# Kernel tuning notes

Measured on AMD Instinct MI355X. Metric: run time of the kernel, lower is better.

## Reference

```python
import jax, jax.numpy as jnp
import numpy as np

NTOK0, NTOK1 = 2048, 512
EMSIZE = 256
NHID = 1024
B, T = 32, 512


def setup_inputs() -> dict:
    key = jax.random.key(0)
    ks = jax.random.split(key, 12)
    initrange = 0.1
    inp = {
        "tokens0": jax.random.randint(ks[0], (B, T), 0, NTOK0),
        "tokens1": jax.random.randint(ks[1], (B, T), 0, NTOK1),
        "h0": jnp.zeros((B, NHID), jnp.float32),
        "c0": jnp.zeros((B, NHID), jnp.float32),
        # embeddings (uniform init as in init_weights)
        "emb0": jax.random.uniform(ks[2], (NTOK0, EMSIZE), jnp.float32, -initrange, initrange),
        "emb1": jax.random.uniform(ks[3], (NTOK1, EMSIZE), jnp.float32, -initrange, initrange),
        # LSTMCell params (PyTorch layout: gates stacked [i, f, g, o])
        "W_ih": jax.random.normal(ks[4], (4 * NHID, 2 * EMSIZE), jnp.float32) * 0.03,
        "W_hh": jax.random.normal(ks[5], (4 * NHID, NHID), jnp.float32) * 0.03,
        "b_ih": jnp.zeros((4 * NHID,), jnp.float32),
        "b_hh": jnp.zeros((4 * NHID,), jnp.float32),
        # per-channel decoders
        "Wd0": jax.random.uniform(ks[6], (NTOK0, NHID), jnp.float32, -initrange, initrange),
        "bd0": jnp.zeros((NTOK0,), jnp.float32),
        "Wd1": jax.random.uniform(ks[7], (NTOK1, NHID), jnp.float32, -initrange, initrange),
        "bd1": jnp.zeros((NTOK1,), jnp.float32),
    }
    return inp


def _lstm_scan(x_bte, h0, c0, W_ih, W_hh, b_ih, b_hh):
    # x_bte: [B, T, 2*EMSIZE] -> scan over time
    def step(carry, x_t):
        h, c = carry
        gates = x_t @ W_ih.T + b_ih + h @ W_hh.T + b_hh  # [B, 4*NHID]
        i, f, g, o = jnp.split(gates, 4, axis=-1)
        i = jax.nn.sigmoid(i)
        f = jax.nn.sigmoid(f)
        g = jnp.tanh(g)
        o = jax.nn.sigmoid(o)
        c = f * c + i * g
        h = o * jnp.tanh(c)
        return (h, c), h

    (h, c), hs = jax.lax.scan(step, (h0, c0), jnp.transpose(x_bte, (1, 0, 2)))
    return jnp.transpose(hs, (1, 0, 2)), h, c  # [B, T, NHID]


def reference(tokens0, tokens1, h0, c0, emb0, emb1, W_ih, W_hh, b_ih, b_hh, Wd0, bd0, Wd1, bd1):
    # encode each channel and concat along feature dim (dropout=0 / eval mode)
    x = jnp.concatenate([emb0[tokens0], emb1[tokens1]], axis=-1)  # [B, T, 2*EMSIZE]
    hs, h_t, c_t = _lstm_scan(x, h0, c0, W_ih, W_hh, b_ih, b_hh)
    dec0 = hs @ Wd0.T + bd0  # [B, T, NTOK0]
    dec1 = hs @ Wd1.T + bd1  # [B, T, NTOK1]
    return dec0, dec1, h_t, c_t
```

## Files before the change

### kernel.cpp

```cpp
#include <hip/hip_runtime.h>

#define DI __device__ __forceinline__

typedef __attribute__((ext_vector_type(8))) short s16x8;
typedef __attribute__((ext_vector_type(4))) float f32x4;

constexpr int BB = 32, TT = 512, NH = 1024, NG = 4096, KX = 512, KT = 1536;
constexpr int NT0 = 2048, NT1 = 512;

constexpr size_t OFF_DEC1 = (size_t)BB * TT * NT0;
constexpr size_t OFF_H    = OFF_DEC1 + (size_t)BB * TT * NT1;
constexpr size_t OFF_C    = OFF_H + (size_t)BB * NH;

constexpr size_t WS_WCAT = 0;
constexpr size_t WS_WD0  = WS_WCAT + (size_t)NG * KT * 2;
constexpr size_t WS_WD1  = WS_WD0 + (size_t)NT0 * NH * 2;
constexpr size_t WS_XE   = WS_WD1 + (size_t)NT1 * NH * 2;
constexpr size_t WS_HSX  = WS_XE + (size_t)TT * BB * KX * 2;
constexpr size_t WS_BIAS = WS_HSX + (size_t)(TT + 1) * BB * NH * 2;
constexpr size_t WS_CNT  = WS_BIAS + (size_t)NG * 4;

DI unsigned short f2bf(float f) {
  unsigned u = __float_as_uint(f);
  u += 0x7fffu + ((u >> 16) & 1u);
  return (unsigned short)(u >> 16);
}

DI s16x8 load16_cp(const unsigned short* p) {
  s16x8 d;
  asm volatile("global_load_dwordx4 %0, %1, off sc0 sc1" : "=v"(d) : "v"(p) : "memory");
  return d;
}
DI void store4_cp(unsigned* p, unsigned v) {
  asm volatile("global_store_dword %0, %1, off sc0 sc1" :: "v"(p), "v"(v) : "memory");
}


__global__ __launch_bounds__(256) void k_wcat(const float* __restrict__ Wih,
                                              const float* __restrict__ Whh,
                                              unsigned short* __restrict__ Wcat) {
  int n = blockIdx.x;
  for (int k = threadIdx.x; k < KT; k += 256) {
    float v = (k < KX) ? Wih[(size_t)n * KX + k] : Whh[(size_t)n * NH + (k - KX)];
    Wcat[(size_t)n * KT + k] = f2bf(v);
  }
}

__global__ __launch_bounds__(256) void k_wd(const float* __restrict__ Wd0,
                                            const float* __restrict__ Wd1,
                                            unsigned short* __restrict__ Wd0b,
                                            unsigned short* __restrict__ Wd1b) {
  int bid = blockIdx.x;
  const float* src;
  unsigned short* dst;
  if (bid < NT0) { src = Wd0 + (size_t)bid * NH; dst = Wd0b + (size_t)bid * NH; }
  else           { src = Wd1 + (size_t)(bid - NT0) * NH; dst = Wd1b + (size_t)(bid - NT0) * NH; }
  for (int k = threadIdx.x; k < NH; k += 256) dst[k] = f2bf(src[k]);
}

__global__ __launch_bounds__(256) void k_misc(const float* __restrict__ bih,
                                              const float* __restrict__ bhh,
                                              const float* __restrict__ h0,
                                              float* __restrict__ bias,
                                              unsigned short* __restrict__ hsx,
                                              unsigned* __restrict__ cnt) {
  int i = blockIdx.x * 256 + threadIdx.x;
  if (i < NG) bias[i] = bih[i] + bhh[i];
  else if (i < NG + BB * NH) { int j = i - NG; hsx[j] = f2bf(h0[j]); }
  else if (i == NG + BB * NH) *cnt = 0u;
}

__global__ __launch_bounds__(64) void k_embed(const int* __restrict__ tok0,
                                              const int* __restrict__ tok1,
                                              const float* __restrict__ emb0,
                                              const float* __restrict__ emb1,
                                              unsigned short* __restrict__ xe) {
  int r = blockIdx.x;
  int t = r >> 5, b = r & 31;
  int i = threadIdx.x;
  int a0 = tok0[b * TT + t], a1 = tok1[b * TT + t];
  const float4* e0 = (const float4*)(emb0 + (size_t)a0 * 256);
  const float4* e1 = (const float4*)(emb1 + (size_t)a1 * 256);
  float4 v0 = e0[i], v1 = e1[i];
  unsigned short* dst = xe + (size_t)r * KX;
  dst[i * 4 + 0] = f2bf(v0.x); dst[i * 4 + 1] = f2bf(v0.y);
  dst[i * 4 + 2] = f2bf(v0.z); dst[i * 4 + 3] = f2bf(v0.w);
  dst[256 + i * 4 + 0] = f2bf(v1.x); dst[256 + i * 4 + 1] = f2bf(v1.y);
  dst[256 + i * 4 + 2] = f2bf(v1.z); dst[256 + i * 4 + 3] = f2bf(v1.w);
}

__global__ __launch_bounds__(256, 1) void k_lstm(const unsigned short* __restrict__ xe,
                                                 const unsigned short* __restrict__ Wcat,
                                                 const float* __restrict__ bias,
                                                 unsigned short* __restrict__ hsx,
                                                 const float* __restrict__ c0,
                                                 float* __restrict__ out_h,
                                                 float* __restrict__ out_c,
                                                 unsigned* cnt) {
  __shared__ char hbuf[65536];
  __shared__ float gbuf[4 * 32 * 17];

  const int tid  = threadIdx.x;
  const int blk  = blockIdx.x;
  const int lane = tid & 63;
  const int g    = tid >> 6;
  const int col  = lane & 15;
  const int kgrp = lane >> 4;
  const int n    = g * NH + blk * 16 + col;
  const float bias_v = bias[n];

  s16x8 wf[48];
  {
    const unsigned short* wbase = Wcat + (size_t)n * KT + kgrp * 8;
    #pragma unroll
    for (int j = 0; j < 48; ++j) wf[j] = *(const s16x8*)(wbase + j * 32);
  }

  const int pb = tid >> 3;
  const int pm = tid & 7;
  const int hid0 = blk * 16 + 2 * pm;
  float c_0 = c0[pb * NH + hid0];
  float c_1 = c0[pb * NH + hid0 + 1];

  const int arow0 = col;
  const int arow1 = 16 + col;
  const int ax0 = (arow0 & 7) << 4;
  const int ax1 = (arow1 & 7) << 4;

  unsigned* hsx32 = (unsigned*)hsx;

  for (int t = 0; t < TT; ++t) {
    const unsigned short* hsrc = hsx + (size_t)t * (BB * NH);
    s16x8 hv[16];
    #pragma unroll
    for (int it = 0; it < 16; ++it) hv[it] = load16_cp(hsrc + (it * 256 + tid) * 8);

    f32x4 acc0 = {bias_v, bias_v, bias_v, bias_v};
    f32x4 acc1 = acc0;
    const unsigned short* x0 = xe + ((size_t)t * BB + arow0) * KX + kgrp * 8;
    const unsigned short* x1 = xe + ((size_t)t * BB + arow1) * KX + kgrp * 8;
    #pragma unroll
    for (int j = 0; j < 16; ++j) {
      s16x8 a0 = *(const s16x8*)(x0 + j * 32);
      acc0 = __builtin_amdgcn_mfma_f32_16x16x32_bf16(a0, wf[j], acc0, 0, 0, 0);
      s16x8 a1 = *(const s16x8*)(x1 + j * 32);
      acc1 = __builtin_amdgcn_mfma_f32_16x16x32_bf16(a1, wf[j], acc1, 0, 0, 0);
    }

    asm volatile("s_waitcnt vmcnt(0)" ::: "memory");
    #pragma unroll
    for (int it = 0; it < 16; ++it) {
      int ch = it * 256 + tid;
      int row = ch >> 7;
      int boff = (ch & 127) << 4;
      *(s16x8*)(hbuf + row * 2048 + (boff ^ ((row & 7) << 4))) = hv[it];
    }
    __syncthreads();

    const char* hb0 = hbuf + arow0 * 2048;
    const char* hb1 = hbuf + arow1 * 2048;
    #pragma unroll
    for (int j = 0; j < 32; ++j) {
      int boff = (j * 32 + kgrp * 8) << 1;
      s16x8 a0 = *(const s16x8*)(hb0 + (boff ^ ax0));
      acc0 = __builtin_amdgcn_mfma_f32_16x16x32_bf16(a0, wf[16 + j], acc0, 0, 0, 0);
      s16x8 a1 = *(const s16x8*)(hb1 + (boff ^ ax1));
      acc1 = __builtin_amdgcn_mfma_f32_16x16x32_bf16(a1, wf[16 + j], acc1, 0, 0, 0);
    }

    #pragma unroll
    for (int i = 0; i < 4; ++i) {
      gbuf[g * 544 + (kgrp * 4 + i) * 17 + col] = acc0[i];
      gbuf[g * 544 + (16 + kgrp * 4 + i) * 17 + col] = acc1[i];
    }
    __syncthreads();

    {
      const float* gb = gbuf + pb * 17 + 2 * pm;
      float gi0 = gb[0 * 544], gi1 = gb[0 * 544 + 1];
      float gf0 = gb[1 * 544], gf1 = gb[1 * 544 + 1];
      float gg0 = gb[2 * 544], gg1 = gb[2 * 544 + 1];
      float go0 = gb[3 * 544], go1 = gb[3 * 544 + 1];
      float iv0 = 1.f / (1.f + __expf(-gi0)), iv1 = 1.f / (1.f + __expf(-gi1));
      float fv0 = 1.f / (1.f + __expf(-gf0)), fv1 = 1.f / (1.f + __expf(-gf1));
      float gv0 = tanhf(gg0),                 gv1 = tanhf(gg1);
      float ov0 = 1.f / (1.f + __expf(-go0)), ov1 = 1.f / (1.f + __expf(-go1));
      c_0 = fv0 * c_0 + iv0 * gv0;
      c_1 = fv1 * c_1 + iv1 * gv1;
      float h0v = ov0 * tanhf(c_0);
      float h1v = ov1 * tanhf(c_1);
      unsigned pk = (unsigned)f2bf(h0v) | ((unsigned)f2bf(h1v) << 16);
      store4_cp(hsx32 + (((size_t)(t + 1) * (BB * NH) + pb * NH + hid0) >> 1), pk);
      if (t == TT - 1) {
        out_h[pb * NH + hid0] = h0v;  out_h[pb * NH + hid0 + 1] = h1v;
        out_c[pb * NH + hid0] = c_0;  out_c[pb * NH + hid0 + 1] = c_1;
      }
    }

    if (t < TT - 1) {
      asm volatile("s_waitcnt vmcnt(0)" ::: "memory");
      __syncthreads();
      if (tid == 0) {
        __hip_atomic_fetch_add(cnt, 1u, __ATOMIC_RELAXED, __HIP_MEMORY_SCOPE_AGENT);
        while (__hip_atomic_load(cnt, __ATOMIC_RELAXED, __HIP_MEMORY_SCOPE_AGENT) <
               (unsigned)gridDim.x * (unsigned)(t + 1))
          __builtin_amdgcn_s_sleep(2);
      }
      __syncthreads();
    }
  }
}


__global__ __launch_bounds__(256) void k_dec(const unsigned short* __restrict__ A,
                                             const unsigned short* __restrict__ Wb,
                                             const float* __restrict__ bd,
                                             float* __restrict__ out, int N, int gn) {
  __shared__ char smem[32768];
  const int tid = threadIdx.x;
  const int bid = blockIdx.x;
  const int tm = bid / gn, tn = bid % gn;
  const int lane = tid & 63;
  const int w = tid >> 6;
  const int wr = w >> 1, wc = w & 1;
  const int col = lane & 15, kgrp = lane >> 4;

  f32x4 acc[4][4];
  #pragma unroll
  for (int i = 0; i < 4; ++i)
    #pragma unroll
    for (int j = 0; j < 4; ++j) acc[i][j] = {0.f, 0.f, 0.f, 0.f};

  const unsigned short* Ag = A + (size_t)(tm * 128) * NH;
  const unsigned short* Bg = Wb + (size_t)(tn * 128) * NH;

  for (int kb = 0; kb < 16; ++kb) {
    #pragma unroll
    for (int it = 0; it < 4; ++it) {
      int ch = it * 256 + tid;
      int row = ch >> 3;
      int ko = (ch & 7) << 3;
      int lo = row * 128 + ((ko << 1) ^ ((row & 7) << 4));
      *(s16x8*)(smem + lo)         = *(const s16x8*)(Ag + (size_t)row * NH + kb * 64 + ko);
      *(s16x8*)(smem + 16384 + lo) = *(const s16x8*)(Bg + (size_t)row * NH + kb * 64 + ko);
    }
    __syncthreads();
    #pragma unroll
    for (int kk = 0; kk < 64; kk += 32) {
      s16x8 av[4], bv[4];
      #pragma unroll
      for (int mi = 0; mi < 4; ++mi) {
        int row = wr * 64 + mi * 16 + col;
        av[mi] = *(const s16x8*)(smem + row * 128 + (((kk + kgrp * 8) << 1) ^ ((row & 7) << 4)));
      }
      #pragma unroll
      for (int ni = 0; ni < 4; ++ni) {
        int row = wc * 64 + ni * 16 + col;
        bv[ni] = *(const s16x8*)(smem + 16384 + row * 128 + (((kk + kgrp * 8) << 1) ^ ((row & 7) << 4)));
      }
      #pragma unroll
      for (int mi = 0; mi < 4; ++mi)
        #pragma unroll
        for (int ni = 0; ni < 4; ++ni)
          acc[mi][ni] = __builtin_amdgcn_mfma_f32_16x16x32_bf16(av[mi], bv[ni], acc[mi][ni], 0, 0, 0);
    }
    __syncthreads();
  }

  #pragma unroll
  for (int ni = 0; ni < 4; ++ni) {
    int nn = tn * 128 + wc * 64 + ni * 16 + col;
    float bv = bd[nn];
    #pragma unroll
    for (int mi = 0; mi < 4; ++mi) {
      #pragma unroll
      for (int i = 0; i < 4; ++i) {
        int r = tm * 128 + wr * 64 + mi * 16 + kgrp * 4 + i;
        int t = r >> 5, b = r & 31;
        out[((size_t)b * TT + t) * N + nn] = acc[mi][ni][i] + bv;
      }
    }
  }
}


extern "C" void kernel_launch(void* const* d_in, const int* in_sizes, int n_in,
                              void* d_out, int out_size, void* d_ws, size_t ws_size,
                              hipStream_t stream) {
  const int*   tok0 = (const int*)d_in[0];
  const int*   tok1 = (const int*)d_in[1];
  const float* h0   = (const float*)d_in[2];
  const float* c0   = (const float*)d_in[3];
  const float* emb0 = (const float*)d_in[4];
  const float* emb1 = (const float*)d_in[5];
  const float* Wih  = (const float*)d_in[6];
  const float* Whh  = (const float*)d_in[7];
  const float* bih  = (const float*)d_in[8];
  const float* bhh  = (const float*)d_in[9];
  const float* Wd0  = (const float*)d_in[10];
  const float* bd0  = (const float*)d_in[11];
  const float* Wd1  = (const float*)d_in[12];
  const float* bd1  = (const float*)d_in[13];

  unsigned char* ws = (unsigned char*)d_ws;
  unsigned short* Wcat = (unsigned short*)(ws + WS_WCAT);
  unsigned short* Wd0b = (unsigned short*)(ws + WS_WD0);
  unsigned short* Wd1b = (unsigned short*)(ws + WS_WD1);
  unsigned short* xe   = (unsigned short*)(ws + WS_XE);
  unsigned short* hsx  = (unsigned short*)(ws + WS_HSX);
  float* bias = (float*)(ws + WS_BIAS);
  unsigned* cnt = (unsigned*)(ws + WS_CNT);
  float* out = (float*)d_out;

  k_wcat<<<NG, 256, 0, stream>>>(Wih, Whh, Wcat);
  k_wd<<<NT0 + NT1, 256, 0, stream>>>(Wd0, Wd1, Wd0b, Wd1b);
  k_misc<<<145, 256, 0, stream>>>(bih, bhh, h0, bias, hsx, cnt);
  k_embed<<<TT * BB, 64, 0, stream>>>(tok0, tok1, emb0, emb1, xe);
  k_lstm<<<64, 256, 0, stream>>>(xe, Wcat, bias, hsx, c0, out + OFF_H, out + OFF_C, cnt);
  k_dec<<<128 * 16, 256, 0, stream>>>(hsx + BB * NH, Wd0b, bd0, out, NT0, 16);
  k_dec<<<128 * 4, 256, 0, stream>>>(hsx + BB * NH, Wd1b, bd1, out + OFF_DEC1, NT1, 4);
}
```

Baseline: 5.187 ms.

## Replace atomic grid barrier with flag-based barrier and overlap next-step input GEMM

Replaces the single atomic counter grid barrier with per-block arrival flags that one master wavefront polls before writing a release flag. The input-projection MFMAs for step t+1 run between arrival and waiting, which hides them in barrier latency. Sigmoid and tanh now use fast reciprocal/exp forms instead of division and tanhf, trading a little accuracy for shorter activation latency. The master-polling barrier adds a serialized hop but avoids atomic contention.

```diff
diff --git a/kernel.cpp b/kernel.cpp
--- a/kernel.cpp
+++ b/kernel.cpp
@@ -18,7 +18,7 @@
 constexpr size_t WS_XE   = WS_WD1 + (size_t)NT1 * NH * 2;
 constexpr size_t WS_HSX  = WS_XE + (size_t)TT * BB * KX * 2;
 constexpr size_t WS_BIAS = WS_HSX + (size_t)(TT + 1) * BB * NH * 2;
-constexpr size_t WS_CNT  = WS_BIAS + (size_t)NG * 4;
+constexpr size_t WS_FLG  = WS_BIAS + (size_t)NG * 4;
 
 DI unsigned short f2bf(float f) {
   unsigned u = __float_as_uint(f);
@@ -34,6 +34,15 @@
 DI void store4_cp(unsigned* p, unsigned v) {
   asm volatile("global_store_dword %0, %1, off sc0 sc1" :: "v"(p), "v"(v) : "memory");
 }
+DI unsigned load4_cp_wait(const unsigned* p) {
+  unsigned d;
+  asm volatile("global_load_dword %0, %1, off sc0 sc1" : "=v"(d) : "v"(p) : "memory");
+  asm volatile("s_waitcnt vmcnt(0)" ::: "memory");
+  return d;
+}
+
+DI float fsig(float x)  { return __builtin_amdgcn_rcpf(1.f + __expf(-x)); }
+DI float ftanh(float x) { return 1.f - 2.f * __builtin_amdgcn_rcpf(1.f + __expf(2.f * x)); }
 
 
 __global__ __launch_bounds__(256) void k_wcat(const float* __restrict__ Wih,
@@ -63,11 +72,11 @@
                                               const float* __restrict__ h0,
                                               float* __restrict__ bias,
                                               unsigned short* __restrict__ hsx,
-                                              unsigned* __restrict__ cnt) {
+                                              unsigned* __restrict__ flags) {
   int i = blockIdx.x * 256 + threadIdx.x;
   if (i < NG) bias[i] = bih[i] + bhh[i];
   else if (i < NG + BB * NH) { int j = i - NG; hsx[j] = f2bf(h0[j]); }
-  else if (i == NG + BB * NH) *cnt = 0u;
+  else if (i < NG + BB * NH + 2112) flags[i - (NG + BB * NH)] = 0u;
 }
 
 __global__ __launch_bounds__(64) void k_embed(const int* __restrict__ tok0,
@@ -96,18 +105,22 @@
                                                  const float* __restrict__ c0,
                                                  float* __restrict__ out_h,
                                                  float* __restrict__ out_c,
-                                                 unsigned* cnt) {
+                                                 unsigned* flags) {
   __shared__ char hbuf[65536];
   __shared__ float gbuf[4 * 32 * 17];
 
   const int tid  = threadIdx.x;
   const int blk  = blockIdx.x;
   const int lane = tid & 63;
-  const int g    = tid >> 6;
+  const int w    = tid >> 6;
+  const int g    = w;
   const int col  = lane & 15;
   const int kgrp = lane >> 4;
   const int n    = g * NH + blk * 16 + col;
   const float bias_v = bias[n];
+
+  unsigned* const arr = flags;
+  unsigned* const rel = flags + 2048;
 
   s16x8 wf[48];
   {
@@ -129,23 +142,28 @@
 
   unsigned* hsx32 = (unsigned*)hsx;
 
+  auto xpart = [&](int tt, f32x4& a0, f32x4& a1) {
+    const unsigned short* xp0 = xe + ((size_t)tt * BB + arow0) * KX + kgrp * 8;
+    const unsigned short* xp1 = xp0 + 16 * KX;
+    a0 = f32x4{bias_v, bias_v, bias_v, bias_v};
+    a1 = a0;
+    #pragma unroll
+    for (int j = 0; j < 16; ++j) {
+      s16x8 b0 = *(const s16x8*)(xp0 + j * 32);
+      a0 = __builtin_amdgcn_mfma_f32_16x16x32_bf16(b0, wf[j], a0, 0, 0, 0);
+      s16x8 b1 = *(const s16x8*)(xp1 + j * 32);
+      a1 = __builtin_amdgcn_mfma_f32_16x16x32_bf16(b1, wf[j], a1, 0, 0, 0);
+    }
+  };
+
+  f32x4 xacc0, xacc1;
+  xpart(0, xacc0, xacc1);
+
   for (int t = 0; t < TT; ++t) {
     const unsigned short* hsrc = hsx + (size_t)t * (BB * NH);
     s16x8 hv[16];
     #pragma unroll
     for (int it = 0; it < 16; ++it) hv[it] = load16_cp(hsrc + (it * 256 + tid) * 8);
-
-    f32x4 acc0 = {bias_v, bias_v, bias_v, bias_v};
-    f32x4 acc1 = acc0;
-    const unsigned short* x0 = xe + ((size_t)t * BB + arow0) * KX + kgrp * 8;
-    const unsigned short* x1 = xe + ((size_t)t * BB + arow1) * KX + kgrp * 8;
-    #pragma unroll
-    for (int j = 0; j < 16; ++j) {
-      s16x8 a0 = *(const s16x8*)(x0 + j * 32);
-      acc0 = __builtin_amdgcn_mfma_f32_16x16x32_bf16(a0, wf[j], acc0, 0, 0, 0);
-      s16x8 a1 = *(const s16x8*)(x1 + j * 32);
-      acc1 = __builtin_amdgcn_mfma_f32_16x16x32_bf16(a1, wf[j], acc1, 0, 0, 0);
-    }
 
     asm volatile("s_waitcnt vmcnt(0)" ::: "memory");
     #pragma unroll
@@ -157,6 +175,7 @@
     }
     __syncthreads();
 
+    f32x4 acc0 = xacc0, acc1 = xacc1;
     const char* hb0 = hbuf + arow0 * 2048;
     const char* hb1 = hbuf + arow1 * 2048;
     #pragma unroll
@@ -181,14 +200,14 @@
       float gf0 = gb[1 * 544], gf1 = gb[1 * 544 + 1];
       float gg0 = gb[2 * 544], gg1 = gb[2 * 544 + 1];
       float go0 = gb[3 * 544], go1 = gb[3 * 544 + 1];
-      float iv0 = 1.f / (1.f + __expf(-gi0)), iv1 = 1.f / (1.f + __expf(-gi1));
-      float fv0 = 1.f / (1.f + __expf(-gf0)), fv1 = 1.f / (1.f + __expf(-gf1));
-      float gv0 = tanhf(gg0),                 gv1 = tanhf(gg1);
-      float ov0 = 1.f / (1.f + __expf(-go0)), ov1 = 1.f / (1.f + __expf(-go1));
+      float iv0 = fsig(gi0), iv1 = fsig(gi1);
+      float fv0 = fsig(gf0), fv1 = fsig(gf1);
+      float gv0 = ftanh(gg0), gv1 = ftanh(gg1);
+      float ov0 = fsig(go0), ov1 = fsig(go1);
       c_0 = fv0 * c_0 + iv0 * gv0;
       c_1 = fv1 * c_1 + iv1 * gv1;
-      float h0v = ov0 * tanhf(c_0);
-      float h1v = ov1 * tanhf(c_1);
+      float h0v = ov0 * ftanh(c_0);
+      float h1v = ov1 * ftanh(c_1);
       unsigned pk = (unsigned)f2bf(h0v) | ((unsigned)f2bf(h1v) << 16);
       store4_cp(hsx32 + (((size_t)(t + 1) * (BB * NH) + pb * NH + hid0) >> 1), pk);
       if (t == TT - 1) {
@@ -198,13 +217,23 @@
     }
 
     if (t < TT - 1) {
+      const unsigned tv = (unsigned)(t + 1);
       asm volatile("s_waitcnt vmcnt(0)" ::: "memory");
       __syncthreads();
+      if (tid == 0) store4_cp(arr + blk * 32, tv);
+
+      xpart(t + 1, xacc0, xacc1);
+
+      if (blk == 0 && w == 0) {
+        const unsigned* ap = arr + lane * 32;
+        for (;;) {
+          unsigned v = load4_cp_wait(ap);
+          if (__all((int)(v >= tv))) break;
+        }
+        if (lane == 0) store4_cp(rel, tv);
+      }
       if (tid == 0) {
-        __hip_atomic_fetch_add(cnt, 1u, __ATOMIC_RELAXED, __HIP_MEMORY_SCOPE_AGENT);
-        while (__hip_atomic_load(cnt, __ATOMIC_RELAXED, __HIP_MEMORY_SCOPE_AGENT) <
-               (unsigned)gridDim.x * (unsigned)(t + 1))
-          __builtin_amdgcn_s_sleep(2);
+        while (load4_cp_wait(rel) < tv) __builtin_amdgcn_s_sleep(1);
       }
       __syncthreads();
     }
@@ -309,14 +338,14 @@
   unsigned short* xe   = (unsigned short*)(ws + WS_XE);
   unsigned short* hsx  = (unsigned short*)(ws + WS_HSX);
   float* bias = (float*)(ws + WS_BIAS);
-  unsigned* cnt = (unsigned*)(ws + WS_CNT);
+  unsigned* flags = (unsigned*)(ws + WS_FLG);
   float* out = (float*)d_out;
 
   k_wcat<<<NG, 256, 0, stream>>>(Wih, Whh, Wcat);
   k_wd<<<NT0 + NT1, 256, 0, stream>>>(Wd0, Wd1, Wd0b, Wd1b);
-  k_misc<<<145, 256, 0, stream>>>(bih, bhh, h0, bias, hsx, cnt);
+  k_misc<<<160, 256, 0, stream>>>(bih, bhh, h0, bias, hsx, flags);
   k_embed<<<TT * BB, 64, 0, stream>>>(tok0, tok1, emb0, emb1, xe);
-  k_lstm<<<64, 256, 0, stream>>>(xe, Wcat, bias, hsx, c0, out + OFF_H, out + OFF_C, cnt);
+  k_lstm<<<64, 256, 0, stream>>>(xe, Wcat, bias, hsx, c0, out + OFF_H, out + OFF_C, flags);
   k_dec<<<128 * 16, 256, 0, stream>>>(hsx + BB * NH, Wd0b, bd0, out, NT0, 16);
   k_dec<<<128 * 4, 256, 0, stream>>>(hsx + BB * NH, Wd1b, bd1, out + OFF_DEC1, NT1, 4);
 }
```

New measurement: 5.558 ms. 1.07x slower.
